# Optimization experiments

Hardware: AMD Instinct MI355X
Metric: run time of the kernel (lower is better)

Reference implementation:

```python
import jax, jax.numpy as jnp
import numpy as np

N_EXPERTS = 8
TOP_K = 2


def setup_inputs() -> dict:
    key = jax.random.key(0)
    k1, k2, k3, k4 = jax.random.split(key, 4)
    B, T, C, H, E = 2, 2048, 1024, 4096, N_EXPERTS
    x = jax.random.normal(k1, (B, T, C), dtype=jnp.float32)
    # weights scaled like standard init to keep activations well-behaved
    router_w = jax.random.normal(k2, (E, C), dtype=jnp.float32) * 0.02
    w1 = jax.random.normal(k3, (E, C, H), dtype=jnp.float32) * (1.0 / np.sqrt(C))
    w2 = jax.random.normal(k4, (E, H, C), dtype=jnp.float32) * (1.0 / np.sqrt(H))
    return {"x": x, "router_w": router_w, "w1": w1, "w2": w2}


def reference(x, router_w, w1, w2):
    B, T, C = x.shape
    E = N_EXPERTS
    xf = x.reshape(-1, C)                                   # [N, C], N = B*T
    logits = jnp.einsum('nc,ec->ne', xf, router_w)          # router (no bias)
    probs = jax.nn.softmax(logits, axis=-1)
    top_w, top_i = jax.lax.top_k(probs, TOP_K)              # [N, K]
    top_w = top_w / jnp.sum(top_w, axis=-1, keepdims=True)  # renormalize
    # combine weight per (token, expert): sum of top-k weights routed to e
    comb = jnp.einsum('nk,nke->ne', top_w, jax.nn.one_hot(top_i, E, dtype=xf.dtype))
    # dense all-expert compute (bias=False, exact GELU, dropout=0 at eval)
    h = jax.nn.gelu(jnp.einsum('nc,ech->enh', xf, w1), approximate=False)  # [E, N, H]
    y = jnp.einsum('enh,ehc->enc', h, w2)                   # [E, N, C]
    out = jnp.einsum('ne,enc->nc', comb, y)                 # weighted combine
    return out.reshape(B, T, C)
```

## Files before the change

kernel.cpp:

```cpp
#include <hip/hip_runtime.h>
#include <hip/hip_bf16.h>
#include <stdint.h>

#define NTOK 4096
#define CD   1024
#define HD   4096
#define NE   8

typedef __attribute__((ext_vector_type(8))) short bf16x8;
typedef __attribute__((ext_vector_type(4))) float f32x4;
typedef __attribute__((ext_vector_type(4))) unsigned short us4;

#define BARR() asm volatile("s_barrier" ::: "memory")
#define VM2() asm volatile("s_waitcnt vmcnt(2)" ::: "memory")
#define VM0() asm volatile("s_waitcnt vmcnt(0)" ::: "memory")

__device__ __forceinline__ unsigned short f2bf(float f){
  __hip_bfloat16 h = __float2bfloat16(f);
  return *reinterpret_cast<unsigned short*>(&h);
}

__global__ __launch_bounds__(256) void router_kernel(
    const float* __restrict__ x, const float* __restrict__ rw,
    unsigned short* __restrict__ x_bf, int* __restrict__ top_i,
    float* __restrict__ top_w, int* __restrict__ counts){
  __shared__ float rw_lds[NE*CD];
  int tid = threadIdx.x;
  for (int i = tid; i < NE*CD/4; i += 256)
    ((float4*)rw_lds)[i] = ((const float4*)rw)[i];
  __syncthreads();
  int l = tid & 63, w = tid >> 6;
  int n = blockIdx.x*4 + w;

  float4 xv[4];
  #pragma unroll
  for (int j = 0; j < 4; ++j)
    xv[j] = ((const float4*)(x + (size_t)n*CD))[l + j*64];

  #pragma unroll
  for (int j = 0; j < 4; ++j){
    us4 o; o.x = f2bf(xv[j].x); o.y = f2bf(xv[j].y); o.z = f2bf(xv[j].z); o.w = f2bf(xv[j].w);
    *(us4*)(x_bf + (size_t)n*CD + l*4 + j*256) = o;
  }

  double le[NE];
  #pragma unroll
  for (int e = 0; e < NE; ++e){
    double p = 0.0;
    #pragma unroll
    for (int j = 0; j < 4; ++j){
      float4 rv = ((const float4*)(rw_lds + e*CD))[l + j*64];
      p += (double)xv[j].x*rv.x + (double)xv[j].y*rv.y + (double)xv[j].z*rv.z + (double)xv[j].w*rv.w;
    }
    #pragma unroll
    for (int d = 32; d >= 1; d >>= 1) p += __shfl_xor(p, d);
    le[e] = p;
  }
  if (l == 0){
    double m = le[0];
    #pragma unroll
    for (int e = 1; e < NE; ++e) m = le[e] > m ? le[e] : m;
    double pe[NE];
    #pragma unroll
    for (int e = 0; e < NE; ++e) pe[e] = exp(le[e]-m);
    int i0 = 0;
    #pragma unroll
    for (int e = 1; e < NE; ++e) if (pe[e] > pe[i0]) i0 = e;
    int i1 = (i0 == 0) ? 1 : 0;
    #pragma unroll
    for (int e = 0; e < NE; ++e){ if (e == i0) continue; if (pe[e] > pe[i1]) i1 = e; }
    double w0 = pe[i0], w1v = pe[i1], wsum = w0 + w1v;
    top_i[2*n] = i0; top_i[2*n+1] = i1;
    top_w[2*n] = (float)(w0/wsum); top_w[2*n+1] = (float)(w1v/wsum);
    atomicAdd(&counts[i0], 1); atomicAdd(&counts[i1], 1);
  }
}

__global__ void scan_kernel(const int* __restrict__ counts, int* __restrict__ offsets, int* __restrict__ cursor){
  if (threadIdx.x == 0){
    int s = 0;
    for (int e = 0; e < NE; ++e){ offsets[e] = s; cursor[e] = s; s += counts[e]; }
  }
}

__global__ __launch_bounds__(256) void scatter_kernel(
    const int* __restrict__ top_i, const float* __restrict__ top_w,
    int* __restrict__ cursor, int* __restrict__ g_tok, float* __restrict__ g_w){
  int n = blockIdx.x*256 + threadIdx.x;
  #pragma unroll
  for (int k = 0; k < 2; ++k){
    int e = top_i[2*n+k];
    int pos = atomicAdd(&cursor[e], 1);
    g_tok[pos] = n;
    g_w[pos] = top_w[2*n+k];
  }
}

template<int R, int S>
__global__ __launch_bounds__(256) void transpose_cvt(const float* __restrict__ in, unsigned short* __restrict__ outp){
  __shared__ float tile[64][65];
  int e = blockIdx.z;
  const float* ip = in + (size_t)e*R*S;
  unsigned short* op = outp + (size_t)e*R*S;
  int s0 = blockIdx.x*64, r0 = blockIdx.y*64;
  int tid = threadIdx.x;
  #pragma unroll
  for (int i = 0; i < 4; ++i){
    int lin = i*256 + tid;
    int rr = lin >> 4, c4 = lin & 15;
    float4 v = *(const float4*)(ip + (size_t)(r0+rr)*S + s0 + c4*4);
    tile[rr][c4*4+0] = v.x; tile[rr][c4*4+1] = v.y;
    tile[rr][c4*4+2] = v.z; tile[rr][c4*4+3] = v.w;
  }
  __syncthreads();
  #pragma unroll
  for (int i = 0; i < 4; ++i){
    int lin = i*256 + tid;
    int ss = lin >> 4, rq = lin & 15;
    us4 o;
    o.x = f2bf(tile[rq*4+0][ss]);
    o.y = f2bf(tile[rq*4+1][ss]);
    o.z = f2bf(tile[rq*4+2][ss]);
    o.w = f2bf(tile[rq*4+3][ss]);
    *(us4*)(op + (size_t)(s0+ss)*R + r0 + rq*4) = o;
  }
}

template<int KLEN, int SPLITK, int EPI>
__global__ __launch_bounds__(512, 6) void gemm_ring3(
    const unsigned short* __restrict__ A_src,
    const unsigned short* __restrict__ B_src,
    unsigned short* __restrict__ h_out,
    float* __restrict__ outp,
    const int* __restrict__ g_tok,
    const float* __restrict__ g_w,
    const int* __restrict__ counts,
    const int* __restrict__ offsets,
    int NDIM, int KSTRIDE){
  constexpr int NT = KLEN/32;
  __shared__ alignas(128) char lds[49152];

  int z = blockIdx.z;
  int e  = (SPLITK == 1) ? z : (z / SPLITK);
  int kz = (SPLITK == 1) ? 0 : (z % SPLITK);
  int n_e = counts[e];
  int m0 = blockIdx.y*128;
  if (m0 >= n_e) return;
  int n0 = blockIdx.x*128;
  int g_base = offsets[e];
  int kstart = kz*KLEN;

  int tid = threadIdx.x, l = tid & 63, w = tid >> 6;
  int wr = w >> 2, wc = w & 3;
  int lrow = l & 15, q = l >> 4;

  const unsigned short* src[2];
  uint32_t dst[2];
  #pragma unroll
  for (int i = 0; i < 2; ++i){
    int g = i*512 + tid;
    bool isA = g < 512;
    int gg = isA ? g : (g - 512);
    int row = gg >> 2, c = gg & 3;
    int cs = c ^ (row & 3);
    if (isA){
      int rg = m0 + row; if (rg > n_e-1) rg = n_e-1;
      size_t arow;
      if (EPI == 0) arow = (size_t)g_tok[g_base + rg];
      else          arow = (size_t)(g_base + rg);
      src[i] = A_src + arow*(size_t)KSTRIDE + kstart + cs*8;
    } else {
      src[i] = B_src + ((size_t)e*NDIM + n0 + row)*(size_t)KSTRIDE + kstart + cs*8;
    }
    dst[i] = (uint32_t)g*16u;
  }

  auto STAGE = [&](int t, uint32_t bufoff){
    #pragma unroll
    for (int i = 0; i < 2; ++i)
      __builtin_amdgcn_global_load_lds(
        (const __attribute__((address_space(1))) void*)(src[i] + (size_t)t*32),
        (__attribute__((address_space(3))) void*)&lds[dst[i] + bufoff], 16, 0, 0);
  };

  uint32_t a_off[4], b_off[2];
  #pragma unroll
  for (int m = 0; m < 4; ++m){
    int ra = wr*64 + m*16 + lrow;
    a_off[m] = (uint32_t)(ra*64) + 16u*(q ^ (ra & 3));
  }
  #pragma unroll
  for (int n = 0; n < 2; ++n){
    int rb = wc*32 + n*16 + lrow;
    b_off[n] = 8192u + (uint32_t)(rb*64) + 16u*(q ^ (rb & 3));
  }

  f32x4 acc[4][2] = {};

  STAGE(0, 0u); STAGE(1, 16384u);

  uint32_t ro = 0u;
  uint32_t so = 32768u;
  #pragma unroll 1
  for (int kt = 0; kt < NT; ++kt){
    if (kt < NT-1) { VM2(); } else { VM0(); }
    BARR();
    if (kt + 2 < NT) STAGE(kt + 2, so);
    bf16x8 av[4], bv[2];
    #pragma unroll
    for (int m = 0; m < 4; ++m)
      av[m] = *(const bf16x8*)&lds[a_off[m] + ro];
    #pragma unroll
    for (int n = 0; n < 2; ++n)
      bv[n] = *(const bf16x8*)&lds[b_off[n] + ro];
    __builtin_amdgcn_s_setprio(1);
    #pragma unroll
    for (int m = 0; m < 4; ++m)
      #pragma unroll
      for (int n = 0; n < 2; ++n)
        acc[m][n] = __builtin_amdgcn_mfma_f32_16x16x32_bf16(av[m], bv[n], acc[m][n], 0, 0, 0);
    __builtin_amdgcn_s_setprio(0);
    ro = (ro == 32768u) ? 0u : ro + 16384u;
    so = (so == 32768u) ? 0u : so + 16384u;
  }

  if (EPI == 0){
    #pragma unroll
    for (int m = 0; m < 4; ++m){
      #pragma unroll
      for (int j = 0; j < 4; ++j){
        int r = m0 + wr*64 + m*16 + q*4 + j;
        if (r < n_e){
          unsigned short* hp = h_out + (size_t)(g_base + r)*NDIM + n0 + wc*32 + lrow;
          #pragma unroll
          for (int n = 0; n < 2; ++n){
            float v = acc[m][n][j];
            v = 0.5f*v*(1.0f + erff(v*0.70710678118654752f));
            hp[n*16] = f2bf(v);
          }
        }
      }
    }
  } else {
    #pragma unroll
    for (int m = 0; m < 4; ++m){
      #pragma unroll
      for (int j = 0; j < 4; ++j){
        int r = m0 + wr*64 + m*16 + q*4 + j;
        if (r < n_e){
          int slot = g_base + r;
          int t = g_tok[slot];
          float wgt = g_w[slot];
          float* op = outp + (size_t)t*NDIM + n0 + wc*32 + lrow;
          #pragma unroll
          for (int n = 0; n < 2; ++n)
            atomicAdd(op + n*16, wgt*acc[m][n][j]);
        }
      }
    }
  }
}

extern "C" void kernel_launch(void* const* d_in, const int* in_sizes, int n_in,
                              void* d_out, int out_size, void* d_ws, size_t ws_size,
                              hipStream_t stream) {
  const float* x  = (const float*)d_in[0];
  const float* rw = (const float*)d_in[1];
  const float* w1 = (const float*)d_in[2];
  const float* w2 = (const float*)d_in[3];

  size_t off = 0;
  auto alloc = [&](size_t sz) -> char* {
    char* p = (char*)d_ws + off;
    off += (sz + 255) & ~(size_t)255;
    return p;
  };
  unsigned short* x_bf = (unsigned short*)alloc((size_t)NTOK*CD*2);
  unsigned short* w1t  = (unsigned short*)alloc((size_t)NE*CD*HD*2);
  unsigned short* w2t  = (unsigned short*)alloc((size_t)NE*CD*HD*2);
  unsigned short* hbuf = (unsigned short*)alloc((size_t)NTOK*2*HD*2);
  int*   top_i  = (int*)alloc(NTOK*2*4);
  float* top_w  = (float*)alloc(NTOK*2*4);
  int*   counts = (int*)alloc(64);
  int*   offs   = (int*)alloc(64);
  int*   cursor = (int*)alloc(64);
  int*   g_tok  = (int*)alloc(NTOK*2*4);
  float* g_w    = (float*)alloc(NTOK*2*4);
  (void)ws_size; (void)in_sizes; (void)n_in; (void)out_size;

  hipMemsetAsync(d_out, 0, (size_t)NTOK*CD*4, stream);
  hipMemsetAsync(counts, 0, 64, stream);

  router_kernel<<<dim3(NTOK/4), dim3(256), 0, stream>>>(x, rw, x_bf, top_i, top_w, counts);
  scan_kernel<<<dim3(1), dim3(64), 0, stream>>>(counts, offs, cursor);
  scatter_kernel<<<dim3(NTOK/256), dim3(256), 0, stream>>>(top_i, top_w, cursor, g_tok, g_w);

  transpose_cvt<CD, HD><<<dim3(HD/64, CD/64, NE), dim3(256), 0, stream>>>(w1, w1t);
  transpose_cvt<HD, CD><<<dim3(CD/64, HD/64, NE), dim3(256), 0, stream>>>(w2, w2t);

  gemm_ring3<CD, 1, 0><<<dim3(HD/128, 12, NE), dim3(512), 0, stream>>>(
      x_bf, w1t, hbuf, (float*)nullptr, g_tok, g_w, counts, offs, HD, CD);
  gemm_ring3<HD/2, 2, 1><<<dim3(CD/128, 12, NE*2), dim3(512), 0, stream>>>(
      hbuf, w2t, (unsigned short*)nullptr, (float*)d_out, g_tok, g_w, counts, offs, CD, HD);
}
```

Before: 457.9 us.

## Remap grouped GEMM block order across XCDs and raise second GEMM split-K to four

```diff
diff --git a/kernel.cpp b/kernel.cpp
--- a/kernel.cpp
+++ b/kernel.cpp
@@ -140,13 +140,19 @@
   constexpr int NT = KLEN/32;
   __shared__ alignas(128) char lds[49152];
 
-  int z = blockIdx.z;
+  int GN = gridDim.x, GY = gridDim.y;
+  int p  = blockIdx.x + GN*(blockIdx.y + GY*blockIdx.z);
+  int k8 = p & 7, qq = p >> 3;
+  int t  = qq / GY, y = qq % GY;
+  int j  = k8 + 8*t;
+  int xb = j % GN, z = j / GN;
+
   int e  = (SPLITK == 1) ? z : (z / SPLITK);
   int kz = (SPLITK == 1) ? 0 : (z % SPLITK);
   int n_e = counts[e];
-  int m0 = blockIdx.y*128;
+  int m0 = y*128;
   if (m0 >= n_e) return;
-  int n0 = blockIdx.x*128;
+  int n0 = xb*128;
   int g_base = offsets[e];
   int kstart = kz*KLEN;
 
@@ -175,11 +181,11 @@
     dst[i] = (uint32_t)g*16u;
   }
 
-  auto STAGE = [&](int t, uint32_t bufoff){
+  auto STAGE = [&](int tt, uint32_t bufoff){
     #pragma unroll
     for (int i = 0; i < 2; ++i)
       __builtin_amdgcn_global_load_lds(
-        (const __attribute__((address_space(1))) void*)(src[i] + (size_t)t*32),
+        (const __attribute__((address_space(1))) void*)(src[i] + (size_t)tt*32),
         (__attribute__((address_space(3))) void*)&lds[dst[i] + bufoff], 16, 0, 0);
   };
 
@@ -228,13 +234,13 @@
     #pragma unroll
     for (int m = 0; m < 4; ++m){
       #pragma unroll
-      for (int j = 0; j < 4; ++j){
-        int r = m0 + wr*64 + m*16 + q*4 + j;
+      for (int jj = 0; jj < 4; ++jj){
+        int r = m0 + wr*64 + m*16 + q*4 + jj;
         if (r < n_e){
           unsigned short* hp = h_out + (size_t)(g_base + r)*NDIM + n0 + wc*32 + lrow;
           #pragma unroll
           for (int n = 0; n < 2; ++n){
-            float v = acc[m][n][j];
+            float v = acc[m][n][jj];
             v = 0.5f*v*(1.0f + erff(v*0.70710678118654752f));
             hp[n*16] = f2bf(v);
           }
@@ -245,16 +251,16 @@
     #pragma unroll
     for (int m = 0; m < 4; ++m){
       #pragma unroll
-      for (int j = 0; j < 4; ++j){
-        int r = m0 + wr*64 + m*16 + q*4 + j;
+      for (int jj = 0; jj < 4; ++jj){
+        int r = m0 + wr*64 + m*16 + q*4 + jj;
         if (r < n_e){
           int slot = g_base + r;
-          int t = g_tok[slot];
+          int tt = g_tok[slot];
           float wgt = g_w[slot];
-          float* op = outp + (size_t)t*NDIM + n0 + wc*32 + lrow;
+          float* op = outp + (size_t)tt*NDIM + n0 + wc*32 + lrow;
           #pragma unroll
           for (int n = 0; n < 2; ++n)
-            atomicAdd(op + n*16, wgt*acc[m][n][j]);
+            atomicAdd(op + n*16, wgt*acc[m][n][jj]);
         }
       }
     }
@@ -300,6 +306,6 @@
 
   gemm_ring3<CD, 1, 0><<<dim3(HD/128, 12, NE), dim3(512), 0, stream>>>(
       x_bf, w1t, hbuf, (float*)nullptr, g_tok, g_w, counts, offs, HD, CD);
-  gemm_ring3<HD/2, 2, 1><<<dim3(CD/128, 12, NE*2), dim3(512), 0, stream>>>(
+  gemm_ring3<HD/4, 4, 1><<<dim3(CD/128, 12, NE*4), dim3(512), 0, stream>>>(
       hbuf, w2t, (unsigned short*)nullptr, (float*)d_out, g_tok, g_w, counts, offs, CD, HD);
 }
```

After: 485.0 us. 5.9% more time.
